# Kernel optimization log

Hardware: AMD Instinct MI355X
Metric: run time of the kernel (lower is better)

The kernel has to match this reference:

```python
import jax, jax.numpy as jnp
import numpy as np

SR = 16000
WIN_LENGTH = int(round(SR / 1000.0 * 25))   # 400 samples
HOP_LENGTH = int(round(SR / 1000.0 * 10))   # 160 samples
EPSILON = 1e-12


def _hamming_window(n):
    # torch.hamming_window(n, periodic=True): 0.54 - 0.46*cos(2*pi*k/n)
    k = jnp.arange(n, dtype=jnp.float32)
    return 0.54 - 0.46 * jnp.cos(2.0 * jnp.pi * k / n)


def _fit_window(win, n_fft):
    # Replicates the module's pad-to / crop-to n_fft logic (static shapes).
    L = win.shape[0]
    if L < n_fft:
        pad = n_fft - L
        b = pad // 2
        win = jnp.concatenate([jnp.zeros(b, win.dtype), win, jnp.zeros(pad - b, win.dtype)])
    elif L > n_fft:
        c = (L - n_fft) // 2
        win = win[c:c + n_fft]
    return win


def setup_inputs() -> dict:
    key = jax.random.key(0)
    # (batch, time_step, n_fft//2 + 1, 2) real/imag onesided STFT
    x = jax.random.normal(key, (16, 3000, 201, 2), dtype=jnp.float32)
    return {"x": x}


def reference(x):
    B, T, F, _ = x.shape
    n_fft = 2 * (F - 1)                       # onesided=True
    xc = jax.lax.complex(x[..., 0], x[..., 1])
    # torch.irfft(..., normalized=False, onesided=True) == numpy-style irfft
    q = jnp.fft.irfft(xc, n=n_fft, axis=-1).astype(x.dtype)   # [B, T, n_fft]
    win = _fit_window(_hamming_window(WIN_LENGTH), n_fft)
    q = q * win
    est_len = (T - 1) * HOP_LENGTH + n_fft
    # Fused overlap-add via a single scatter-add instead of a per-frame loop.
    idx = jnp.arange(T)[:, None] * HOP_LENGTH + jnp.arange(n_fft)[None, :]  # [T, n_fft]
    istft = jnp.zeros((B, est_len), x.dtype).at[:, idx].add(q)
    sq_win = win * win
    ssw = jnp.zeros((est_len,), x.dtype).at[idx].add(jnp.broadcast_to(sq_win, (T, n_fft)))
    istft = jnp.where(ssw > EPSILON, istft / ssw, istft)
    # center=True: trim n_fft//2 on each side
    istft = istft[:, n_fft // 2: est_len - n_fft // 2]
    return istft
```

## Files before the change

### kernel.cpp

```cpp
#include <hip/hip_runtime.h>
#include <hip/hip_bf16.h>
#include <math.h>

constexpr int BB     = 16;
constexpr int T      = 3000;
constexpr int F      = 201;
constexpr int NFFT   = 400;
constexpr int HOP    = 160;
constexpr int K      = 402;
constexpr int ESTLEN = (T - 1) * HOP + NFFT;
constexpr int OUTLEN = ESTLEN - NFFT;
constexpr float EPS  = 1e-12f;

constexpr int WJ    = 416;
constexpr int WSTEP = WJ * 32;
constexpr int NSTEP = 13;
constexpr int UT    = 64;

typedef short bf16x8 __attribute__((ext_vector_type(8)));
typedef float f32x16 __attribute__((ext_vector_type(16)));

__device__ __forceinline__ unsigned short f2bf(float f) {
    unsigned int u = __float_as_uint(f);
    u = (u + 0x7fffu + ((u >> 16) & 1u)) >> 16;
    return (unsigned short)u;
}

__global__ void build_wt(unsigned short* __restrict__ Wg) {
    int idx = blockIdx.x * blockDim.x + threadIdx.x;
    if (idx >= NSTEP * WSTEP) return;
    int ksg = idx / WSTEP;
    int rem = idx - ksg * WSTEP;
    int j  = rem >> 5;
    int kk = rem & 31;
    int sp = kk >> 3;
    int ww = kk & 7;
    int s  = sp ^ (j & 3);
    float v = 0.f;
    if (j < NFFT) {
        int k = -1;
        if (ksg == 12 && s >= 2) {
            if (s == 2 && ww >= 6) k = 394 + ww;
        } else {
            k = ksg * 32 + s * 8 + ww;
        }
        if (k >= 0 && k < K) {
            int f = k >> 1;
            bool is_re = (k & 1) == 0;
            float c = (f == 0 || f == F - 1) ? (1.f / 400.f) : (2.f / 400.f);
            int m = (j * f) % NFFT;
            float ang = (float)(2.0 * M_PI * (double)m / 400.0);
            float tw = is_re ? cosf(ang) : -sinf(ang);
            float win = 0.54f - 0.46f * cosf((float)(2.0 * M_PI * (double)j / 400.0));
            v = c * tw * win;
        }
    }
    Wg[idx] = f2bf(v);
}

__global__ void build_rssw(float* __restrict__ rssw) {
    int p = blockIdx.x * blockDim.x + threadIdx.x;
    if (p >= ESTLEN) return;
    int t_hi = p / HOP; if (t_hi > T - 1) t_hi = T - 1;
    int t_lo = (p >= NFFT) ? ((p - NFFT) / HOP + 1) : 0;
    float s = 0.f;
    for (int t = t_lo; t <= t_hi; ++t) {
        int j = p - t * HOP;
        float w = 0.54f - 0.46f * cosf((float)(2.0 * M_PI * (double)j / 400.0));
        s += w * w;
    }
    rssw[p] = (s > EPS) ? 1.f / s : 1.f;
}

__global__ __launch_bounds__(256, 3)
void istft_fused(const float* __restrict__ A, const unsigned short* __restrict__ Wg,
                 const float* __restrict__ rssw, const float* __restrict__ zpage,
                 float* __restrict__ out) {
    __shared__ unsigned short Ws[2 * WSTEP];

    const int tid  = threadIdx.x;
    const int lane = tid & 63;
    const int w    = tid >> 6;
    const int kh   = w >> 1;
    const int wu   = w & 1;
    const int lj   = lane & 31;
    const int lh   = lane >> 5;
    const int b    = blockIdx.y;
    const int u0   = 1 + blockIdx.x * UT;

    f32x16 acc[5];
    #pragma unroll
    for (int mf = 0; mf < 5; ++mf)
        #pragma unroll
        for (int q = 0; q < 16; ++q) acc[mf][q] = 0.f;

    const float* pdt[3];
    #pragma unroll
    for (int dt = 0; dt < 3; ++dt) {
        int t = u0 + wu * 32 + lj - dt;
        pdt[dt] = (t >= 0 && t < T) ? (A + (size_t)(b * T + t) * K) : zpage;
    }

    auto issue_W = [&](unsigned short* dst, int ksg) {
        const unsigned short* sb = Wg + (size_t)ksg * WSTEP;
        #pragma unroll
        for (int p = 0; p < 7; ++p) {
            int P = p * 256 + tid;
            if (P < WJ * 4) {
                __builtin_amdgcn_global_load_lds(
                    (const __attribute__((address_space(1))) void*)(sb + (size_t)P * 8),
                    (__attribute__((address_space(3))) void*)(dst + (p * 256 + w * 64) * 8),
                    16, 0, 0);
            }
        }
    };

    auto aofs = [&](int s) -> int {
        return (s == 12 && kh == 1) ? 394 : s * 32 + kh * 16 + lh * 8;
    };
    auto loadA = [&](int s, float2* d) {
        int o = aofs(s);
        #pragma unroll
        for (int dt = 0; dt < 3; ++dt) {
            const float* p = pdt[dt] + o;
            #pragma unroll
            for (int q = 0; q < 4; ++q)
                d[dt * 4 + q] = *reinterpret_cast<const float2*>(p + 2 * q);
        }
    };

    float2 a2c[12], a2n[12];

    loadA(0, a2c);
    issue_W(&Ws[0], 0);
    __syncthreads();

    const int spl = (kh * 2 + lh) ^ (lj & 3);

    for (int s = 0; s < NSTEP; ++s) {
        const unsigned short* Wb = &Ws[(s & 1) * WSTEP];
        if (s + 1 < NSTEP) {
            issue_W(&Ws[((s + 1) & 1) * WSTEP], s + 1);
            loadA(s + 1, a2n);
        }
        bf16x8 af[3];
        #pragma unroll
        for (int dt = 0; dt < 3; ++dt) {
            union { bf16x8 v; __hip_bfloat162 h[4]; } u;
            #pragma unroll
            for (int q = 0; q < 4; ++q)
                u.h[q] = __float22bfloat162_rn(
                    make_float2(a2c[dt * 4 + q].x, a2c[dt * 4 + q].y));
            af[dt] = u.v;
        }
        #pragma unroll
        for (int dt = 0; dt < 3; ++dt) {
            const int nmf = (dt < 2) ? 5 : 3;
            #pragma unroll
            for (int mf = 0; mf < 5; ++mf) {
                if (mf < nmf) {
                    int j = dt * 160 + mf * 32 + lj;
                    bf16x8 bf = *reinterpret_cast<const bf16x8*>(&Wb[j * 32 + spl * 8]);
                    acc[mf] = __builtin_amdgcn_mfma_f32_32x32x16_bf16(
                        af[dt], bf, acc[mf], 0, 0, 0);
                }
            }
        }
        __syncthreads();
        if (s + 1 < NSTEP) {
            #pragma unroll
            for (int i = 0; i < 12; ++i) a2c[i] = a2n[i];
        }
    }

    float* xch = reinterpret_cast<float*>(Ws);
    if (kh == 1) {
        #pragma unroll
        for (int mf = 0; mf < 5; ++mf) {
            int base = ((wu * 5 + mf) * 64 + lane) * 16;
            #pragma unroll
            for (int q = 0; q < 4; ++q)
                *reinterpret_cast<float4*>(&xch[base + q * 4]) =
                    make_float4(acc[mf][q * 4], acc[mf][q * 4 + 1],
                                acc[mf][q * 4 + 2], acc[mf][q * 4 + 3]);
        }
    }
    __syncthreads();
    if (kh == 0) {
        #pragma unroll
        for (int mf = 0; mf < 5; ++mf) {
            int base = ((wu * 5 + mf) * 64 + lane) * 16;
            float part[16];
            #pragma unroll
            for (int q = 0; q < 4; ++q) {
                float4 v = *reinterpret_cast<const float4*>(&xch[base + q * 4]);
                part[q * 4] = v.x; part[q * 4 + 1] = v.y;
                part[q * 4 + 2] = v.z; part[q * 4 + 3] = v.w;
            }
            int m = mf * 32 + lj;
            #pragma unroll
            for (int rg = 0; rg < 16; ++rg) {
                int u  = u0 + wu * 32 + (rg & 3) + 8 * (rg >> 2) + 4 * lh;
                int pe = u * HOP + m;
                int po = pe - (NFFT / 2);
                if (po >= 0 && po < OUTLEN)
                    out[(size_t)b * OUTLEN + po] = (acc[mf][rg] + part[rg]) * rssw[pe];
            }
        }
    }
}

extern "C" void kernel_launch(void* const* d_in, const int* in_sizes, int n_in,
                              void* d_out, int out_size, void* d_ws, size_t ws_size,
                              hipStream_t stream) {
    const float* x = (const float*)d_in[0];
    float* out = (float*)d_out;

    char* ws = (char*)d_ws;
    unsigned short* Wg = (unsigned short*)ws;
    float* rssw = (float*)(ws + 346112);
    float* zpage = (float*)(ws + 346112 + 1920960);

    hipMemsetAsync(zpage, 0, 2048, stream);
    {
        int total = NSTEP * WSTEP;
        build_wt<<<(total + 255) / 256, 256, 0, stream>>>(Wg);
    }
    {
        build_rssw<<<(ESTLEN + 255) / 256, 256, 0, stream>>>(rssw);
    }
    {
        dim3 grid((T + UT - 1) / UT, BB);
        istft_fused<<<grid, 256, 0, stream>>>(x, Wg, rssw, zpage, out);
    }
}
```

Measured before the change: 77.13 us.

## Stage bf16 A tile in shared memory and widen block to six waves

Input frames are now loaded cooperatively once per k-step, converted to bf16 and stored in a double-buffered, swizzled LDS tile. Each wave then reads its three time-shifted A fragments from LDS instead of issuing three separate global loads per lane. The block grows to 384 threads covering 96 frames (three wave-rows per k-half), which amortizes the W tile loads over more frames. The cost is more LDS per block, which may reduce occupancy, plus a more complex tail handling at k-step 12.

```diff
diff --git a/kernel.cpp b/kernel.cpp
--- a/kernel.cpp
+++ b/kernel.cpp
@@ -15,7 +15,9 @@
 constexpr int WJ    = 416;
 constexpr int WSTEP = WJ * 32;
 constexpr int NSTEP = 13;
-constexpr int UT    = 64;
+constexpr int UT    = 96;
+constexpr int ARR   = 98;
+constexpr int NTHR  = 384;
 
 typedef short bf16x8 __attribute__((ext_vector_type(8)));
 typedef float f32x16 __attribute__((ext_vector_type(16)));
@@ -33,27 +35,20 @@
     int rem = idx - ksg * WSTEP;
     int j  = rem >> 5;
     int kk = rem & 31;
-    int sp = kk >> 3;
-    int ww = kk & 7;
-    int s  = sp ^ (j & 3);
+    int op = kk >> 3;
+    int i  = kk & 7;
+    int ol = op ^ ((j >> 1) & 3);
+    int k  = ksg * 32 + ol * 8 + i;
     float v = 0.f;
-    if (j < NFFT) {
-        int k = -1;
-        if (ksg == 12 && s >= 2) {
-            if (s == 2 && ww >= 6) k = 394 + ww;
-        } else {
-            k = ksg * 32 + s * 8 + ww;
-        }
-        if (k >= 0 && k < K) {
-            int f = k >> 1;
-            bool is_re = (k & 1) == 0;
-            float c = (f == 0 || f == F - 1) ? (1.f / 400.f) : (2.f / 400.f);
-            int m = (j * f) % NFFT;
-            float ang = (float)(2.0 * M_PI * (double)m / 400.0);
-            float tw = is_re ? cosf(ang) : -sinf(ang);
-            float win = 0.54f - 0.46f * cosf((float)(2.0 * M_PI * (double)j / 400.0));
-            v = c * tw * win;
-        }
+    if (j < NFFT && k < K) {
+        int f = k >> 1;
+        bool is_re = (k & 1) == 0;
+        float c = (f == 0 || f == F - 1) ? (1.f / 400.f) : (2.f / 400.f);
+        int m = (j * f) % NFFT;
+        float ang = (float)(2.0 * M_PI * (double)m / 400.0);
+        float tw = is_re ? cosf(ang) : -sinf(ang);
+        float win = 0.54f - 0.46f * cosf((float)(2.0 * M_PI * (double)j / 400.0));
+        v = c * tw * win;
     }
     Wg[idx] = f2bf(v);
 }
@@ -72,21 +67,24 @@
     rssw[p] = (s > EPS) ? 1.f / s : 1.f;
 }
 
-__global__ __launch_bounds__(256, 3)
+__global__ __launch_bounds__(NTHR, 3)
 void istft_fused(const float* __restrict__ A, const unsigned short* __restrict__ Wg,
                  const float* __restrict__ rssw, const float* __restrict__ zpage,
                  float* __restrict__ out) {
-    __shared__ unsigned short Ws[2 * WSTEP];
+    __shared__ __align__(16) unsigned short smem[2 * WSTEP + 2 * ARR * 32];
+    unsigned short* WsBuf = smem;
+    unsigned short* AsBuf = smem + 2 * WSTEP;
 
     const int tid  = threadIdx.x;
     const int lane = tid & 63;
     const int w    = tid >> 6;
-    const int kh   = w >> 1;
-    const int wu   = w & 1;
+    const int kh   = (w >= 3) ? 1 : 0;
+    const int wu   = kh ? (w - 3) : w;
     const int lj   = lane & 31;
     const int lh   = lane >> 5;
     const int b    = blockIdx.y;
     const int u0   = 1 + blockIdx.x * UT;
+    const int tbase = u0 - 2;
 
     f32x16 acc[5];
     #pragma unroll
@@ -94,64 +92,90 @@
         #pragma unroll
         for (int q = 0; q < 16; ++q) acc[mf][q] = 0.f;
 
-    const float* pdt[3];
-    #pragma unroll
-    for (int dt = 0; dt < 3; ++dt) {
-        int t = u0 + wu * 32 + lj - dt;
-        pdt[dt] = (t >= 0 && t < T) ? (A + (size_t)(b * T + t) * K) : zpage;
-    }
-
-    auto issue_W = [&](unsigned short* dst, int ksg) {
+    const int r0  = tid >> 2, p0 = tid & 3;
+    const int cl0 = p0 ^ ((r0 >> 1) & 3);
+    const int t0  = tbase + r0;
+    const float* arow0 = (t0 >= 0 && t0 < T) ? A + (size_t)(b * T + t0) * K : zpage;
+    const bool has2 = (tid < 8);
+    const int r1  = 96 + (tid >> 2), p1 = tid & 3;
+    const int cl1 = p1 ^ ((r1 >> 1) & 3);
+    const int t1  = tbase + r1;
+    const float* arow1 = (t1 >= 0 && t1 < T) ? A + (size_t)(b * T + t1) * K : zpage;
+
+    auto loadA = [&](int k0, bool tail, float4* d) {
+        if (!tail) {
+            const float* s0 = arow0 + k0 + cl0 * 8;
+            d[0] = *reinterpret_cast<const float4*>(s0);
+            d[1] = *reinterpret_cast<const float4*>(s0 + 4);
+            if (has2) {
+                const float* s1 = arow1 + k0 + cl1 * 8;
+                d[2] = *reinterpret_cast<const float4*>(s1);
+                d[3] = *reinterpret_cast<const float4*>(s1 + 4);
+            }
+        } else {
+            float v0[8], v1[8];
+            #pragma unroll
+            for (int i = 0; i < 8; ++i) {
+                int ka = k0 + cl0 * 8 + i;
+                v0[i] = (ka < K) ? arow0[ka] : 0.f;
+            }
+            d[0] = make_float4(v0[0], v0[1], v0[2], v0[3]);
+            d[1] = make_float4(v0[4], v0[5], v0[6], v0[7]);
+            if (has2) {
+                #pragma unroll
+                for (int i = 0; i < 8; ++i) {
+                    int ka = k0 + cl1 * 8 + i;
+                    v1[i] = (ka < K) ? arow1[ka] : 0.f;
+                }
+                d[2] = make_float4(v1[0], v1[1], v1[2], v1[3]);
+                d[3] = make_float4(v1[4], v1[5], v1[6], v1[7]);
+            }
+        }
+    };
+
+    auto writeA = [&](unsigned short* dst, const float4* d) {
+        union { bf16x8 v; __hip_bfloat162 h[4]; } u;
+        u.h[0] = __float22bfloat162_rn(make_float2(d[0].x, d[0].y));
+        u.h[1] = __float22bfloat162_rn(make_float2(d[0].z, d[0].w));
+        u.h[2] = __float22bfloat162_rn(make_float2(d[1].x, d[1].y));
+        u.h[3] = __float22bfloat162_rn(make_float2(d[1].z, d[1].w));
+        *reinterpret_cast<bf16x8*>(&dst[r0 * 32 + p0 * 8]) = u.v;
+        if (has2) {
+            union { bf16x8 v; __hip_bfloat162 h[4]; } u2;
+            u2.h[0] = __float22bfloat162_rn(make_float2(d[2].x, d[2].y));
+            u2.h[1] = __float22bfloat162_rn(make_float2(d[2].z, d[2].w));
+            u2.h[2] = __float22bfloat162_rn(make_float2(d[3].x, d[3].y));
+            u2.h[3] = __float22bfloat162_rn(make_float2(d[3].z, d[3].w));
+            *reinterpret_cast<bf16x8*>(&dst[r1 * 32 + p1 * 8]) = u2.v;
+        }
+    };
+
+    auto issueW = [&](unsigned short* dst, int ksg) {
         const unsigned short* sb = Wg + (size_t)ksg * WSTEP;
         #pragma unroll
-        for (int p = 0; p < 7; ++p) {
-            int P = p * 256 + tid;
+        for (int p = 0; p < 5; ++p) {
+            int P = p * NTHR + tid;
             if (P < WJ * 4) {
                 __builtin_amdgcn_global_load_lds(
                     (const __attribute__((address_space(1))) void*)(sb + (size_t)P * 8),
-                    (__attribute__((address_space(3))) void*)(dst + (p * 256 + w * 64) * 8),
+                    (__attribute__((address_space(3))) void*)(dst + (p * NTHR + w * 64) * 8),
                     16, 0, 0);
             }
         }
     };
 
-    auto aofs = [&](int s) -> int {
-        return (s == 12 && kh == 1) ? 394 : s * 32 + kh * 16 + lh * 8;
-    };
-    auto loadA = [&](int s, float2* d) {
-        int o = aofs(s);
+    const int q4  = kh * 2 + lh;
+    const int spl = q4 ^ ((lj >> 1) & 3);
+
+    auto compute = [&](int buf) {
+        const unsigned short* Wb = WsBuf + buf * WSTEP;
+        const unsigned short* Ab = AsBuf + buf * (ARR * 32);
+        bf16x8 af[3];
         #pragma unroll
         for (int dt = 0; dt < 3; ++dt) {
-            const float* p = pdt[dt] + o;
-            #pragma unroll
-            for (int q = 0; q < 4; ++q)
-                d[dt * 4 + q] = *reinterpret_cast<const float2*>(p + 2 * q);
-        }
-    };
-
-    float2 a2c[12], a2n[12];
-
-    loadA(0, a2c);
-    issue_W(&Ws[0], 0);
-    __syncthreads();
-
-    const int spl = (kh * 2 + lh) ^ (lj & 3);
-
-    for (int s = 0; s < NSTEP; ++s) {
-        const unsigned short* Wb = &Ws[(s & 1) * WSTEP];
-        if (s + 1 < NSTEP) {
-            issue_W(&Ws[((s + 1) & 1) * WSTEP], s + 1);
-            loadA(s + 1, a2n);
-        }
-        bf16x8 af[3];
-        #pragma unroll
-        for (int dt = 0; dt < 3; ++dt) {
-            union { bf16x8 v; __hip_bfloat162 h[4]; } u;
-            #pragma unroll
-            for (int q = 0; q < 4; ++q)
-                u.h[q] = __float22bfloat162_rn(
-                    make_float2(a2c[dt * 4 + q].x, a2c[dt * 4 + q].y));
-            af[dt] = u.v;
+            int r  = wu * 32 + lj + 2 - dt;
+            int sl = q4 ^ ((r >> 1) & 3);
+            af[dt] = *reinterpret_cast<const bf16x8*>(&Ab[r * 32 + sl * 8]);
         }
         #pragma unroll
         for (int dt = 0; dt < 3; ++dt) {
@@ -166,14 +190,30 @@
                 }
             }
         }
+    };
+
+    {
+        float4 d[4];
+        loadA(0, false, d);
+        issueW(WsBuf, 0);
+        writeA(AsBuf, d);
         __syncthreads();
-        if (s + 1 < NSTEP) {
-            #pragma unroll
-            for (int i = 0; i < 12; ++i) a2c[i] = a2n[i];
-        }
-    }
-
-    float* xch = reinterpret_cast<float*>(Ws);
+    }
+
+    for (int s = 0; s < NSTEP; ++s) {
+        const int cur = s & 1, nxt = cur ^ 1;
+        const bool dn = (s + 1 < NSTEP);
+        float4 d[4];
+        if (dn) {
+            loadA((s + 1) * 32, (s + 1) == 12, d);
+            issueW(WsBuf + nxt * WSTEP, s + 1);
+        }
+        compute(cur);
+        if (dn) writeA(AsBuf + nxt * (ARR * 32), d);
+        __syncthreads();
+    }
+
+    float* xch = reinterpret_cast<float*>(smem);
     if (kh == 1) {
         #pragma unroll
         for (int mf = 0; mf < 5; ++mf) {
@@ -231,6 +271,6 @@
     }
     {
         dim3 grid((T + UT - 1) / UT, BB);
-        istft_fused<<<grid, 256, 0, stream>>>(x, Wg, rssw, zpage, out);
-    }
-}
+        istft_fused<<<grid, NTHR, 0, stream>>>(x, Wg, rssw, zpage, out);
+    }
+}
```

After: 71.83 us. 1.07x faster.

## Restructure iSTFT GEMM to single-wave blocks with register-resident weight fragments

Applied to the files above, without the earlier changes.

The fused kernel now runs one 64-thread wave per block instead of four waves that split K and had to reduce partial sums through LDS. The twiddle/window matrix is pre-laid out in MFMA fragment order, so each lane loads its bf16 B fragments straight from global/L2 into registers. Only the frame data A is staged, as bf16, in a double-buffered LDS tile. Each wave covers both 32-frame halves, reusing each weight fragment for two MFMAs and removing the cross-wave reduction and block barriers. The cost is more global weight traffic per block, since every block rereads the whole weight matrix from cache. It also uses more registers per thread (two accumulator sets plus 13 weight fragments), which may limit occupancy.

```diff
diff --git a/kernel.cpp b/kernel.cpp
--- a/kernel.cpp
+++ b/kernel.cpp
@@ -12,10 +12,11 @@
 constexpr int OUTLEN = ESTLEN - NFFT;
 constexpr float EPS  = 1e-12f;
 
-constexpr int WJ    = 416;
-constexpr int WSTEP = WJ * 32;
-constexpr int NSTEP = 13;
-constexpr int UT    = 64;
+constexpr int NSTEP  = 26;
+constexpr int NFRAG  = 13;
+constexpr int UT     = 64;
+constexpr int AITEMS = 132;
+constexpr int ABUF   = AITEMS * 8;
 
 typedef short bf16x8 __attribute__((ext_vector_type(8)));
 typedef float f32x16 __attribute__((ext_vector_type(16)));
@@ -28,32 +29,27 @@
 
 __global__ void build_wt(unsigned short* __restrict__ Wg) {
     int idx = blockIdx.x * blockDim.x + threadIdx.x;
-    if (idx >= NSTEP * WSTEP) return;
-    int ksg = idx / WSTEP;
-    int rem = idx - ksg * WSTEP;
-    int j  = rem >> 5;
-    int kk = rem & 31;
-    int sp = kk >> 3;
-    int ww = kk & 7;
-    int s  = sp ^ (j & 3);
+    if (idx >= NSTEP * NFRAG * 512) return;
+    int fid = idx >> 9;
+    int rem = idx & 511;
+    int l = rem >> 3;
+    int e = rem & 7;
+    int s = fid / NFRAG;
+    int f = fid - s * NFRAG;
+    int dt = (f < 5) ? 0 : ((f < 10) ? 1 : 2);
+    int mf = f - dt * 5;
+    int j  = dt * 160 + mf * 32 + (l & 31);
+    int k  = s * 16 + (l >> 5) * 8 + e;
     float v = 0.f;
-    if (j < NFFT) {
-        int k = -1;
-        if (ksg == 12 && s >= 2) {
-            if (s == 2 && ww >= 6) k = 394 + ww;
-        } else {
-            k = ksg * 32 + s * 8 + ww;
-        }
-        if (k >= 0 && k < K) {
-            int f = k >> 1;
-            bool is_re = (k & 1) == 0;
-            float c = (f == 0 || f == F - 1) ? (1.f / 400.f) : (2.f / 400.f);
-            int m = (j * f) % NFFT;
-            float ang = (float)(2.0 * M_PI * (double)m / 400.0);
-            float tw = is_re ? cosf(ang) : -sinf(ang);
-            float win = 0.54f - 0.46f * cosf((float)(2.0 * M_PI * (double)j / 400.0));
-            v = c * tw * win;
-        }
+    if (j < NFFT && k < K) {
+        int fr = k >> 1;
+        bool is_re = (k & 1) == 0;
+        float c = (fr == 0 || fr == F - 1) ? (1.f / 400.f) : (2.f / 400.f);
+        int m = (j * fr) % NFFT;
+        float ang = (float)(2.0 * M_PI * (double)m / 400.0);
+        float tw = is_re ? cosf(ang) : -sinf(ang);
+        float win = 0.54f - 0.46f * cosf((float)(2.0 * M_PI * (double)j / 400.0));
+        v = c * tw * win;
     }
     Wg[idx] = f2bf(v);
 }
@@ -72,142 +68,130 @@
     rssw[p] = (s > EPS) ? 1.f / s : 1.f;
 }
 
-__global__ __launch_bounds__(256, 3)
+__global__ __launch_bounds__(64)
 void istft_fused(const float* __restrict__ A, const unsigned short* __restrict__ Wg,
                  const float* __restrict__ rssw, const float* __restrict__ zpage,
                  float* __restrict__ out) {
-    __shared__ unsigned short Ws[2 * WSTEP];
-
-    const int tid  = threadIdx.x;
-    const int lane = tid & 63;
-    const int w    = tid >> 6;
-    const int kh   = w >> 1;
-    const int wu   = w & 1;
+    __shared__ __align__(16) unsigned short As[2 * ABUF];
+
+    const int lane = threadIdx.x;
     const int lj   = lane & 31;
     const int lh   = lane >> 5;
     const int b    = blockIdx.y;
     const int u0   = 1 + blockIdx.x * UT;
-
-    f32x16 acc[5];
+    const int tbase = u0 - 2;
+
+    f32x16 acc[2][5];
     #pragma unroll
-    for (int mf = 0; mf < 5; ++mf)
-        #pragma unroll
-        for (int q = 0; q < 16; ++q) acc[mf][q] = 0.f;
-
-    const float* pdt[3];
+    for (int ub = 0; ub < 2; ++ub)
+        #pragma unroll
+        for (int mf = 0; mf < 5; ++mf)
+            #pragma unroll
+            for (int q = 0; q < 16; ++q) acc[ub][mf][q] = 0.f;
+
+    const int h = lane & 1;
+    const float* rp[3];
     #pragma unroll
-    for (int dt = 0; dt < 3; ++dt) {
-        int t = u0 + wu * 32 + lj - dt;
-        pdt[dt] = (t >= 0 && t < T) ? (A + (size_t)(b * T + t) * K) : zpage;
-    }
-
-    auto issue_W = [&](unsigned short* dst, int ksg) {
-        const unsigned short* sb = Wg + (size_t)ksg * WSTEP;
-        #pragma unroll
-        for (int p = 0; p < 7; ++p) {
-            int P = p * 256 + tid;
-            if (P < WJ * 4) {
-                __builtin_amdgcn_global_load_lds(
-                    (const __attribute__((address_space(1))) void*)(sb + (size_t)P * 8),
-                    (__attribute__((address_space(3))) void*)(dst + (p * 256 + w * 64) * 8),
-                    16, 0, 0);
+    for (int q = 0; q < 3; ++q) {
+        int r = q * 32 + (lane >> 1);
+        int t = tbase + r;
+        rp[q] = (t >= 0 && t < T && r < 66) ? (A + (size_t)(b * T + t) * K) : zpage;
+    }
+
+    auto loadA = [&](int k0, float4* d) {
+        if (k0 < 400) {
+            #pragma unroll
+            for (int q = 0; q < 3; ++q) {
+                if (q < 2 || lane < 4) {
+                    const float* s = rp[q] + k0 + h * 8;
+                    d[q * 2]     = *reinterpret_cast<const float4*>(s);
+                    d[q * 2 + 1] = *reinterpret_cast<const float4*>(s + 4);
+                }
+            }
+        } else {
+            #pragma unroll
+            for (int q = 0; q < 3; ++q) {
+                if (q < 2 || lane < 4) {
+                    float2 v = make_float2(0.f, 0.f);
+                    if (h == 0) v = *reinterpret_cast<const float2*>(rp[q] + 400);
+                    d[q * 2]     = make_float4(v.x, v.y, 0.f, 0.f);
+                    d[q * 2 + 1] = make_float4(0.f, 0.f, 0.f, 0.f);
+                }
             }
         }
     };
 
-    auto aofs = [&](int s) -> int {
-        return (s == 12 && kh == 1) ? 394 : s * 32 + kh * 16 + lh * 8;
+    auto writeA = [&](unsigned short* dst, const float4* d) {
+        #pragma unroll
+        for (int q = 0; q < 3; ++q) {
+            if (q < 2 || lane < 4) {
+                int item = q * 64 + lane;
+                union { bf16x8 v; __hip_bfloat162 hh[4]; } u;
+                u.hh[0] = __float22bfloat162_rn(make_float2(d[q*2].x,   d[q*2].y));
+                u.hh[1] = __float22bfloat162_rn(make_float2(d[q*2].z,   d[q*2].w));
+                u.hh[2] = __float22bfloat162_rn(make_float2(d[q*2+1].x, d[q*2+1].y));
+                u.hh[3] = __float22bfloat162_rn(make_float2(d[q*2+1].z, d[q*2+1].w));
+                *reinterpret_cast<bf16x8*>(&dst[item * 8]) = u.v;
+            }
+        }
     };
-    auto loadA = [&](int s, float2* d) {
-        int o = aofs(s);
-        #pragma unroll
-        for (int dt = 0; dt < 3; ++dt) {
-            const float* p = pdt[dt] + o;
-            #pragma unroll
-            for (int q = 0; q < 4; ++q)
-                d[dt * 4 + q] = *reinterpret_cast<const float2*>(p + 2 * q);
-        }
-    };
-
-    float2 a2c[12], a2n[12];
-
-    loadA(0, a2c);
-    issue_W(&Ws[0], 0);
-    __syncthreads();
-
-    const int spl = (kh * 2 + lh) ^ (lj & 3);
+
+    {
+        float4 d[6];
+        loadA(0, d);
+        writeA(As, d);
+    }
 
     for (int s = 0; s < NSTEP; ++s) {
-        const unsigned short* Wb = &Ws[(s & 1) * WSTEP];
-        if (s + 1 < NSTEP) {
-            issue_W(&Ws[((s + 1) & 1) * WSTEP], s + 1);
-            loadA(s + 1, a2n);
-        }
-        bf16x8 af[3];
-        #pragma unroll
-        for (int dt = 0; dt < 3; ++dt) {
-            union { bf16x8 v; __hip_bfloat162 h[4]; } u;
-            #pragma unroll
-            for (int q = 0; q < 4; ++q)
-                u.h[q] = __float22bfloat162_rn(
-                    make_float2(a2c[dt * 4 + q].x, a2c[dt * 4 + q].y));
-            af[dt] = u.v;
-        }
+        const int cur = s & 1;
+        float4 d[6];
+        if (s + 1 < NSTEP) loadA((s + 1) * 16, d);
+
+        const unsigned short* wb = Wg + ((size_t)(s * NFRAG) << 9) + lane * 8;
+        bf16x8 wf[NFRAG];
+        #pragma unroll
+        for (int f = 0; f < NFRAG; ++f)
+            wf[f] = *reinterpret_cast<const bf16x8*>(wb + ((size_t)f << 9));
+
+        const unsigned short* Ab = As + cur * ABUF;
+        bf16x8 af[2][3];
+        #pragma unroll
+        for (int ub = 0; ub < 2; ++ub)
+            #pragma unroll
+            for (int dt = 0; dt < 3; ++dt) {
+                int row = ub * 32 + lj + 2 - dt;
+                af[ub][dt] = *reinterpret_cast<const bf16x8*>(&Ab[(row * 2 + lh) * 8]);
+            }
+
         #pragma unroll
         for (int dt = 0; dt < 3; ++dt) {
             const int nmf = (dt < 2) ? 5 : 3;
             #pragma unroll
-            for (int mf = 0; mf < 5; ++mf) {
-                if (mf < nmf) {
-                    int j = dt * 160 + mf * 32 + lj;
-                    bf16x8 bf = *reinterpret_cast<const bf16x8*>(&Wb[j * 32 + spl * 8]);
-                    acc[mf] = __builtin_amdgcn_mfma_f32_32x32x16_bf16(
-                        af[dt], bf, acc[mf], 0, 0, 0);
-                }
-            }
-        }
-        __syncthreads();
-        if (s + 1 < NSTEP) {
-            #pragma unroll
-            for (int i = 0; i < 12; ++i) a2c[i] = a2n[i];
-        }
-    }
-
-    float* xch = reinterpret_cast<float*>(Ws);
-    if (kh == 1) {
+            for (int mf = 0; mf < 5; ++mf)
+                if (mf < nmf)
+                    #pragma unroll
+                    for (int ub = 0; ub < 2; ++ub)
+                        acc[ub][mf] = __builtin_amdgcn_mfma_f32_32x32x16_bf16(
+                            af[ub][dt], wf[dt * 5 + mf], acc[ub][mf], 0, 0, 0);
+        }
+
+        if (s + 1 < NSTEP) writeA(As + (cur ^ 1) * ABUF, d);
+    }
+
+    #pragma unroll
+    for (int ub = 0; ub < 2; ++ub)
         #pragma unroll
         for (int mf = 0; mf < 5; ++mf) {
-            int base = ((wu * 5 + mf) * 64 + lane) * 16;
-            #pragma unroll
-            for (int q = 0; q < 4; ++q)
-                *reinterpret_cast<float4*>(&xch[base + q * 4]) =
-                    make_float4(acc[mf][q * 4], acc[mf][q * 4 + 1],
-                                acc[mf][q * 4 + 2], acc[mf][q * 4 + 3]);
-        }
-    }
-    __syncthreads();
-    if (kh == 0) {
-        #pragma unroll
-        for (int mf = 0; mf < 5; ++mf) {
-            int base = ((wu * 5 + mf) * 64 + lane) * 16;
-            float part[16];
-            #pragma unroll
-            for (int q = 0; q < 4; ++q) {
-                float4 v = *reinterpret_cast<const float4*>(&xch[base + q * 4]);
-                part[q * 4] = v.x; part[q * 4 + 1] = v.y;
-                part[q * 4 + 2] = v.z; part[q * 4 + 3] = v.w;
-            }
             int m = mf * 32 + lj;
             #pragma unroll
             for (int rg = 0; rg < 16; ++rg) {
-                int u  = u0 + wu * 32 + (rg & 3) + 8 * (rg >> 2) + 4 * lh;
+                int u  = u0 + ub * 32 + (rg & 3) + 8 * (rg >> 2) + 4 * lh;
                 int pe = u * HOP + m;
                 int po = pe - (NFFT / 2);
                 if (po >= 0 && po < OUTLEN)
-                    out[(size_t)b * OUTLEN + po] = (acc[mf][rg] + part[rg]) * rssw[pe];
-            }
-        }
-    }
+                    out[(size_t)b * OUTLEN + po] = acc[ub][mf][rg] * rssw[pe];
+            }
+        }
 }
 
 extern "C" void kernel_launch(void* const* d_in, const int* in_sizes, int n_in,
@@ -218,12 +202,12 @@
 
     char* ws = (char*)d_ws;
     unsigned short* Wg = (unsigned short*)ws;
-    float* rssw = (float*)(ws + 346112);
+    float* rssw  = (float*)(ws + 346112);
     float* zpage = (float*)(ws + 346112 + 1920960);
 
     hipMemsetAsync(zpage, 0, 2048, stream);
     {
-        int total = NSTEP * WSTEP;
+        int total = NSTEP * NFRAG * 512;
         build_wt<<<(total + 255) / 256, 256, 0, stream>>>(Wg);
     }
     {
@@ -231,6 +215,6 @@
     }
     {
         dim3 grid((T + UT - 1) / UT, BB);
-        istft_fused<<<grid, 256, 0, stream>>>(x, Wg, rssw, zpage, out);
-    }
-}
+        istft_fused<<<grid, 64, 0, stream>>>(x, Wg, rssw, zpage, out);
+    }
+}
```

After: 126.0 us. 63.4% more time.
